# Kernel tuning notes

Measured on AMD Instinct MI355X. Metric: run time of the kernel, lower is better.

Reference implementation:

```python
import jax, jax.numpy as jnp
import numpy as np

ALPHA = 1.0
INF = 1e4  # larger than any possible distance in a 256x256 image


def _row_dist_to_zero(x):
    """1D distance along last axis to nearest zero pixel. x: [..., W] (0/1)."""
    W = x.shape[-1]
    idx = jnp.arange(W, dtype=jnp.float32)
    is0 = x == 0
    # nearest zero at-or-before each position
    last0 = jax.lax.cummax(jnp.where(is0, idx, -1.0), axis=x.ndim - 1)
    fwd = jnp.where(last0 >= 0, idx - last0, INF)
    # nearest zero at-or-after each position (suffix max of -idx)
    neg_next0 = jax.lax.cummax(jnp.where(is0, -idx, -INF), axis=x.ndim - 1, reverse=True)
    bwd = jnp.where(neg_next0 > -INF, (-neg_next0) - idx, INF)
    return jnp.minimum(fwd, bwd)


def _edt_2d(target):
    """Exact Euclidean distance transform per [B,C] map: distance from nonzero
    pixels to nearest zero pixel (matches scipy.ndimage.distance_transform_edt)."""
    B, C, H, W = target.shape
    g = _row_dist_to_zero(target)            # [B,C,H,W] distance along width
    g2 = g * g
    i = jnp.arange(H, dtype=jnp.float32)
    dk2 = (i[:, None] - i[None, :]) ** 2     # [H(out), H(k)]
    # dt2[b,c,i,w] = min_k g2[b,c,k,w] + (i-k)^2
    d2 = jnp.min(g2[:, :, None, :, :] + dk2[None, None, :, :, None], axis=3)
    return jnp.sqrt(d2)


def _distance_map(target):
    dist = _edt_2d(target)
    dmax = jnp.max(dist, axis=(-2, -1), keepdims=True)
    return dist / (dmax + 1e-7)


def setup_inputs() -> dict:
    key = jax.random.key(0)
    k1, k2 = jax.random.split(key)
    pred = jax.random.normal(k1, (8, 1, 256, 256), dtype=jnp.float32)
    target = jax.random.randint(k2, (8, 1, 256, 256), 0, 2).astype(jnp.float32)
    return {"pred": pred, "target": target}


def reference(pred, target):
    dist_map = _distance_map(target)
    weight_map = 1.0 + ALPHA * dist_map
    # numerically stable BCE with logits, reduction='none'
    bce = jnp.maximum(pred, 0.0) - pred * target + jnp.log1p(jnp.exp(-jnp.abs(pred)))
    return jnp.mean(weight_map * bce)
```

## Files before the change

kernel.cpp:

```cpp
#include <hip/hip_runtime.h>
#include <math.h>

#define BATCH 8
#define H 256
#define W 256
#define NPIX (BATCH * H * W)
#define CT 4
#define NBLK 512
#define NROWS (BATCH * H)

__device__ __forceinline__ float bce_logits(float p, float t) {
    return fmaxf(p, 0.0f) - p * t + log1pf(expf(-fabsf(p)));
}

__global__ void __launch_bounds__(256) make_masks(const float* __restrict__ target,
                                                  unsigned long long* __restrict__ masks) {
    const int wv = threadIdx.x >> 6, l = threadIdx.x & 63;
    const int r = blockIdx.x * 4 + wv;
    const float* trow = target + (size_t)r * W;
    float t0 = trow[l], t1 = trow[l + 64], t2 = trow[l + 128], t3 = trow[l + 192];
    unsigned long long m0 = __ballot(t0 == 0.0f);
    unsigned long long m1 = __ballot(t1 == 0.0f);
    unsigned long long m2 = __ballot(t2 == 0.0f);
    unsigned long long m3 = __ballot(t3 == 0.0f);
    if (l < 4) {
        unsigned long long m = (l == 0) ? m0 : (l == 1) ? m1 : (l == 2) ? m2 : m3;
        masks[(size_t)r * 4 + l] = m;
    }
}

__global__ void __launch_bounds__(256, 2) edt_bce_main(
        const unsigned long long* __restrict__ masks, const float* __restrict__ pred,
        const float* __restrict__ target,
        float* __restrict__ pmx, float* __restrict__ psb, float* __restrict__ psdb) {
    __shared__ float col[H][CT];
    __shared__ float part[4][H][CT];
    __shared__ float red[3][4];

    const int tid = threadIdx.x;
    const int wv = tid >> 6, l = tid & 63;
    const int b  = blockIdx.x >> 6;
    const int w0 = (blockIdx.x & 63) * CT;

    const size_t off = ((size_t)(b * H + tid)) * W + w0;
    const float4 p4 = *(const float4*)(pred + off);
    const float4 t4 = *(const float4*)(target + off);
    const unsigned long long* mrow = masks + ((size_t)(b * H + tid)) * 4;
    unsigned long long mw0 = mrow[0], mw1 = mrow[1], mw2 = mrow[2], mw3 = mrow[3];

    {
        unsigned long long mw[4] = {mw0, mw1, mw2, mw3};
        #pragma unroll
        for (int c = 0; c < CT; ++c) {
            const int p = w0 + c;
            int best = 1 << 20;
            #pragma unroll
            for (int w = 0; w < 4; ++w) {
                const int rel = p - (w << 6);
                const unsigned long long m = mw[w];
                unsigned long long mlo = (rel < 0)  ? 0ull
                                       : (rel >= 63) ? m : (m & ((2ull << rel) - 1ull));
                unsigned long long mhi = (rel <= 0) ? m
                                       : (rel > 63)  ? 0ull : (m & (~0ull << rel));
                if (mlo) best = min(best, rel - (63 - __builtin_clzll(mlo)));
                if (mhi) best = min(best, __builtin_ctzll(mhi) - rel);
            }
            float d = (best > 255) ? 1e4f : (float)best;
            col[tid][c] = d * d;
        }
    }
    __syncthreads();

    float acc[4][CT];
    #pragma unroll
    for (int j = 0; j < 4; ++j)
        #pragma unroll
        for (int c = 0; c < CT; ++c) acc[j][c] = 3.0e38f;

    const int k0 = wv << 6;
    #pragma unroll 4
    for (int kk = 0; kk < 64; ++kk) {
        const int k = k0 + kk;
        float4 c4 = *(const float4*)&col[k][0];
        float d0 = (float)(l - k);
        #pragma unroll
        for (int j = 0; j < 4; ++j) {
            float dk  = d0 + (float)(64 * j);
            float dk2 = dk * dk;
            acc[j][0] = fminf(acc[j][0], c4.x + dk2);
            acc[j][1] = fminf(acc[j][1], c4.y + dk2);
            acc[j][2] = fminf(acc[j][2], c4.z + dk2);
            acc[j][3] = fminf(acc[j][3], c4.w + dk2);
        }
    }
    #pragma unroll
    for (int j = 0; j < 4; ++j)
        *(float4*)&part[wv][l + 64 * j][0] = *(float4*)&acc[j][0];
    __syncthreads();

    float4 r0 = *(const float4*)&part[0][tid][0];
    float4 r1 = *(const float4*)&part[1][tid][0];
    float4 r2 = *(const float4*)&part[2][tid][0];
    float4 r3 = *(const float4*)&part[3][tid][0];
    float dd0 = fminf(fminf(r0.x, r1.x), fminf(r2.x, r3.x));
    float dd1 = fminf(fminf(r0.y, r1.y), fminf(r2.y, r3.y));
    float dd2 = fminf(fminf(r0.z, r1.z), fminf(r2.z, r3.z));
    float dd3 = fminf(fminf(r0.w, r1.w), fminf(r2.w, r3.w));

    float mx = fmaxf(fmaxf(dd0, dd1), fmaxf(dd2, dd3));
    float b0 = bce_logits(p4.x, t4.x);
    float b1 = bce_logits(p4.y, t4.y);
    float b2 = bce_logits(p4.z, t4.z);
    float b3 = bce_logits(p4.w, t4.w);
    float sb  = (b0 + b1) + (b2 + b3);
    float sdb = (sqrtf(dd0) * b0 + sqrtf(dd1) * b1) + (sqrtf(dd2) * b2 + sqrtf(dd3) * b3);

    #pragma unroll
    for (int o = 32; o > 0; o >>= 1) {
        mx  = fmaxf(mx, __shfl_down(mx, o, 64));
        sb  += __shfl_down(sb, o, 64);
        sdb += __shfl_down(sdb, o, 64);
    }
    if (l == 0) { red[0][wv] = mx; red[1][wv] = sb; red[2][wv] = sdb; }
    __syncthreads();
    if (tid == 0) {
        pmx [blockIdx.x] = fmaxf(fmaxf(red[0][0], red[0][1]), fmaxf(red[0][2], red[0][3]));
        psb [blockIdx.x] = (red[1][0] + red[1][1]) + (red[1][2] + red[1][3]);
        psdb[blockIdx.x] = (red[2][0] + red[2][1]) + (red[2][2] + red[2][3]);
    }
}

__global__ void final_reduce(const float* __restrict__ pmx, const float* __restrict__ psb,
                             const float* __restrict__ psdb, float* __restrict__ out) {
    const int tid = threadIdx.x;
    const int img = tid >> 5, j = tid & 31;
    const int e0 = (img << 6) + j, e1 = e0 + 32;
    float mx  = fmaxf(pmx[e0], pmx[e1]);
    float sb  = psb[e0] + psb[e1];
    float sdb = psdb[e0] + psdb[e1];
    #pragma unroll
    for (int o = 16; o > 0; o >>= 1) {
        mx  = fmaxf(mx, __shfl_down(mx, o, 32));
        sb  += __shfl_down(sb, o, 32);
        sdb += __shfl_down(sdb, o, 32);
    }
    __shared__ float cimg[8], simg[8];
    if (j == 0) {
        cimg[img] = sdb / (sqrtf(mx) + 1e-7f);
        simg[img] = sb;
    }
    __syncthreads();
    if (tid == 0) {
        float tot = 0.0f;
        #pragma unroll
        for (int i = 0; i < 8; ++i) tot += simg[i] + cimg[i];
        out[0] = tot * (1.0f / (float)NPIX);
    }
}

extern "C" void kernel_launch(void* const* d_in, const int* in_sizes, int n_in,
                              void* d_out, int out_size, void* d_ws, size_t ws_size,
                              hipStream_t stream) {
    const float* pred   = (const float*)d_in[0];
    const float* target = (const float*)d_in[1];

    unsigned long long* masks = (unsigned long long*)d_ws;
    float* pmx  = (float*)((char*)d_ws + (size_t)NROWS * 4 * sizeof(unsigned long long));
    float* psb  = pmx + NBLK;
    float* psdb = psb + NBLK;

    make_masks<<<NROWS / 4, 256, 0, stream>>>(target, masks);
    edt_bce_main<<<NBLK, 256, 0, stream>>>(masks, pred, target, pmx, psb, psdb);
    final_reduce<<<1, 256, 0, stream>>>(pmx, psb, psdb, (float*)d_out);
}
```

Baseline: 75.40 us.

## Halve column tile and give each thread a full output row scan

```diff
diff --git a/kernel.cpp b/kernel.cpp
--- a/kernel.cpp
+++ b/kernel.cpp
@@ -5,8 +5,8 @@
 #define H 256
 #define W 256
 #define NPIX (BATCH * H * W)
-#define CT 4
-#define NBLK 512
+#define CT 2
+#define NBLK (BATCH * (W / CT))
 #define NROWS (BATCH * H)
 
 __device__ __forceinline__ float bce_logits(float p, float t) {
@@ -29,27 +29,27 @@
     }
 }
 
-__global__ void __launch_bounds__(256, 2) edt_bce_main(
+__global__ void edt_bce_main(
         const unsigned long long* __restrict__ masks, const float* __restrict__ pred,
         const float* __restrict__ target,
         float* __restrict__ pmx, float* __restrict__ psb, float* __restrict__ psdb) {
-    __shared__ float col[H][CT];
-    __shared__ float part[4][H][CT];
+    __shared__ float2 colv[H];
     __shared__ float red[3][4];
 
     const int tid = threadIdx.x;
     const int wv = tid >> 6, l = tid & 63;
-    const int b  = blockIdx.x >> 6;
-    const int w0 = (blockIdx.x & 63) * CT;
+    const int b  = blockIdx.x >> 7;
+    const int w0 = (blockIdx.x & 127) * CT;
 
     const size_t off = ((size_t)(b * H + tid)) * W + w0;
-    const float4 p4 = *(const float4*)(pred + off);
-    const float4 t4 = *(const float4*)(target + off);
+    const float2 p2 = *(const float2*)(pred + off);
+    const float2 t2 = *(const float2*)(target + off);
     const unsigned long long* mrow = masks + ((size_t)(b * H + tid)) * 4;
     unsigned long long mw0 = mrow[0], mw1 = mrow[1], mw2 = mrow[2], mw3 = mrow[3];
 
     {
         unsigned long long mw[4] = {mw0, mw1, mw2, mw3};
+        float g[CT];
         #pragma unroll
         for (int c = 0; c < CT; ++c) {
             const int p = w0 + c;
@@ -66,54 +66,30 @@
                 if (mhi) best = min(best, __builtin_ctzll(mhi) - rel);
             }
             float d = (best > 255) ? 1e4f : (float)best;
-            col[tid][c] = d * d;
+            g[c] = d * d;
         }
+        colv[tid] = make_float2(g[0], g[1]);
     }
     __syncthreads();
 
-    float acc[4][CT];
-    #pragma unroll
-    for (int j = 0; j < 4; ++j)
-        #pragma unroll
-        for (int c = 0; c < CT; ++c) acc[j][c] = 3.0e38f;
+    const float fi = (float)tid;
+    float acc0 = 3.0e38f, acc1 = 3.0e38f;
+    float fk = 0.0f;
+    #pragma unroll 4
+    for (int k = 0; k < H; k += 2) {
+        float2 cA = colv[k];
+        float2 cB = colv[k + 1];
+        float dA = fi - fk, dB = dA - 1.0f;
+        acc0 = fminf(acc0, fminf(fmaf(dA, dA, cA.x), fmaf(dB, dB, cB.x)));
+        acc1 = fminf(acc1, fminf(fmaf(dA, dA, cA.y), fmaf(dB, dB, cB.y)));
+        fk += 2.0f;
+    }
 
-    const int k0 = wv << 6;
-    #pragma unroll 4
-    for (int kk = 0; kk < 64; ++kk) {
-        const int k = k0 + kk;
-        float4 c4 = *(const float4*)&col[k][0];
-        float d0 = (float)(l - k);
-        #pragma unroll
-        for (int j = 0; j < 4; ++j) {
-            float dk  = d0 + (float)(64 * j);
-            float dk2 = dk * dk;
-            acc[j][0] = fminf(acc[j][0], c4.x + dk2);
-            acc[j][1] = fminf(acc[j][1], c4.y + dk2);
-            acc[j][2] = fminf(acc[j][2], c4.z + dk2);
-            acc[j][3] = fminf(acc[j][3], c4.w + dk2);
-        }
-    }
-    #pragma unroll
-    for (int j = 0; j < 4; ++j)
-        *(float4*)&part[wv][l + 64 * j][0] = *(float4*)&acc[j][0];
-    __syncthreads();
-
-    float4 r0 = *(const float4*)&part[0][tid][0];
-    float4 r1 = *(const float4*)&part[1][tid][0];
-    float4 r2 = *(const float4*)&part[2][tid][0];
-    float4 r3 = *(const float4*)&part[3][tid][0];
-    float dd0 = fminf(fminf(r0.x, r1.x), fminf(r2.x, r3.x));
-    float dd1 = fminf(fminf(r0.y, r1.y), fminf(r2.y, r3.y));
-    float dd2 = fminf(fminf(r0.z, r1.z), fminf(r2.z, r3.z));
-    float dd3 = fminf(fminf(r0.w, r1.w), fminf(r2.w, r3.w));
-
-    float mx = fmaxf(fmaxf(dd0, dd1), fmaxf(dd2, dd3));
-    float b0 = bce_logits(p4.x, t4.x);
-    float b1 = bce_logits(p4.y, t4.y);
-    float b2 = bce_logits(p4.z, t4.z);
-    float b3 = bce_logits(p4.w, t4.w);
-    float sb  = (b0 + b1) + (b2 + b3);
-    float sdb = (sqrtf(dd0) * b0 + sqrtf(dd1) * b1) + (sqrtf(dd2) * b2 + sqrtf(dd3) * b3);
+    float mx = fmaxf(acc0, acc1);
+    float b0 = bce_logits(p2.x, t2.x);
+    float b1 = bce_logits(p2.y, t2.y);
+    float sb  = b0 + b1;
+    float sdb = sqrtf(acc0) * b0 + sqrtf(acc1) * b1;
 
     #pragma unroll
     for (int o = 32; o > 0; o >>= 1) {
@@ -134,10 +110,15 @@
                              const float* __restrict__ psdb, float* __restrict__ out) {
     const int tid = threadIdx.x;
     const int img = tid >> 5, j = tid & 31;
-    const int e0 = (img << 6) + j, e1 = e0 + 32;
-    float mx  = fmaxf(pmx[e0], pmx[e1]);
-    float sb  = psb[e0] + psb[e1];
-    float sdb = psdb[e0] + psdb[e1];
+    const int base = (img << 7) + j;
+    float mx = 0.0f, sb = 0.0f, sdb = 0.0f;
+    #pragma unroll
+    for (int q = 0; q < 4; ++q) {
+        const int e = base + 32 * q;
+        mx  = fmaxf(mx, pmx[e]);
+        sb  += psb[e];
+        sdb += psdb[e];
+    }
     #pragma unroll
     for (int o = 16; o > 0; o >>= 1) {
         mx  = fmaxf(mx, __shfl_down(mx, o, 32));
```

New measurement: 74.51 us. About the same (-1.2%).
